# Kernel tuning notes

Measured on AMD Instinct MI355X. Metric: run time of the kernel, lower is better.

Reference implementation:

```python
import jax, jax.numpy as jnp
import numpy as np
import math

B, S, D, H, DFF = 2, 2048, 1024, 16, 4096
DK = D // H
EPS = 1e-6


def setup_inputs() -> dict:
    key = jax.random.key(0)
    ks = jax.random.split(key, 12)
    s = 0.02
    return {
        "x": jax.random.normal(ks[0], (B, S, D), jnp.float32),
        "mask": jnp.ones((B, S), jnp.int32),
        "wq": jax.random.normal(ks[1], (D, D), jnp.float32) * s,
        "bq": jnp.zeros((D,), jnp.float32),
        "wk": jax.random.normal(ks[2], (D, D), jnp.float32) * s,
        "bk": jnp.zeros((D,), jnp.float32),
        "wv": jax.random.normal(ks[3], (D, D), jnp.float32) * s,
        "bv": jnp.zeros((D,), jnp.float32),
        "wo": jax.random.normal(ks[4], (D, D), jnp.float32) * s,
        "bo": jnp.zeros((D,), jnp.float32),
        "g1": jnp.ones((D,), jnp.float32),
        "b1": jnp.zeros((D,), jnp.float32),
        "g2": jnp.ones((D,), jnp.float32),
        "b2": jnp.zeros((D,), jnp.float32),
        "w1": jax.random.normal(ks[5], (DFF, D), jnp.float32) * s,
        "bf1": jnp.zeros((DFF,), jnp.float32),
        "w2": jax.random.normal(ks[6], (D, DFF), jnp.float32) * s,
        "bf2": jnp.zeros((D,), jnp.float32),
    }


def _gelu(x):
    # x * 0.5 * (1 + erf(x / sqrt(2))) -- exact erf-based GELU as in source
    return x * 0.5 * (1.0 + jax.lax.erf(x * (1.0 / math.sqrt(2.0))))


def _layernorm(x, gamma, beta):
    # torch.std uses unbiased (ddof=1); eps is OUTSIDE the sqrt in the source
    mean = jnp.mean(x, axis=-1, keepdims=True)
    std = jnp.std(x, axis=-1, keepdims=True, ddof=1)
    return gamma * (x - mean) / (std + EPS) + beta


def _block(x, mask, wq, bq, wk, bk, wv, bv, wo, bo, g1, b1, g2, b2, w1, bf1, w2, bf2):
    # multi-head attention (dropout is identity in eval mode)
    q = (x @ wq.T + bq).reshape(B, S, H, DK).transpose(0, 2, 1, 3)  # bhsd
    k = (x @ wk.T + bk).reshape(B, S, H, DK).transpose(0, 2, 1, 3)
    v = (x @ wv.T + bv).reshape(B, S, H, DK).transpose(0, 2, 1, 3)
    scores = jnp.einsum("bhsd,bhtd->bhst", q, k) / math.sqrt(DK)
    scores = jnp.where(mask[:, None, None, :] == 0, -1e9, scores)
    attn = jax.nn.softmax(scores, axis=-1)
    cv = jnp.einsum("bhst,bhtd->bhsd", attn, v)
    cv = cv.transpose(0, 2, 1, 3).reshape(B, S, D)
    hd = cv @ wo.T + bo
    # residual + norm1
    hd = _layernorm(x + hd, g1, b1)
    # position-wise FFN with erf GELU
    ff = _gelu(hd @ w1.T + bf1) @ w2.T + bf2
    return _layernorm(hd + ff, g2, b2)


def reference(x, mask, wq, bq, wk, bk, wv, bv, wo, bo, g1, b1, g2, b2, w1, bf1, w2, bf2):
    return _block(x, mask, wq, bq, wk, bk, wv, bv, wo, bo, g1, b1, g2, b2, w1, bf1, w2, bf2)
```

## Files before the change

kernel.cpp:

```cpp
#include <hip/hip_runtime.h>
#include <hip/hip_bf16.h>

#define B_   2
#define S_   2048
#define D_   1024
#define H_   16
#define DK_  64
#define DFF_ 4096
#define M_   (B_*S_)

typedef unsigned short u16;
typedef __attribute__((ext_vector_type(8))) short short8;
typedef __attribute__((ext_vector_type(4))) short bf16x4;
typedef __attribute__((ext_vector_type(4))) float floatx4;

__device__ __forceinline__ u16 f2bf(float f) {
    union { float f; unsigned u; } v; v.f = f;
    unsigned r = v.u + 0x7fffu + ((v.u >> 16) & 1u);
    return (u16)(r >> 16);
}
__device__ __forceinline__ u16 f2bf_fast(float f) {
    __hip_bfloat16 h = __float2bfloat16(f);
    return *reinterpret_cast<u16*>(&h);
}
__device__ __forceinline__ float exp2_fast(float f) {
    return __builtin_amdgcn_exp2f(f);
}
__device__ __forceinline__ void g2l16(const u16* g, u16* l) {
    __builtin_amdgcn_global_load_lds((const __attribute__((address_space(1))) void*)g,
                                     (__attribute__((address_space(3))) void*)l,
                                     16, 0, 0);
}
__device__ __forceinline__ unsigned lds_off(const void* p) {
    return (unsigned)(unsigned long long)p;
}

#define TRB16(dst, va, IMM)                                                    \
    asm volatile("ds_read_b64_tr_b16 %0, %1 offset:" #IMM                      \
                 : "=v"(dst) : "v"(va))

__global__ __launch_bounds__(256) void cvt_all(
    const float* __restrict__ x,  const float* __restrict__ wq,
    const float* __restrict__ wk, const float* __restrict__ wv,
    const float* __restrict__ wo, const float* __restrict__ w1,
    const float* __restrict__ w2,
    u16* __restrict__ xb, u16* __restrict__ wqkvb, u16* __restrict__ wob,
    u16* __restrict__ w1b, u16* __restrict__ w2b) {
    for (int i = blockIdx.x * 256 + threadIdx.x; i < 4194304;
         i += gridDim.x * 256) {
        const float* s; u16* d; int off;
        if (i < 1048576)      { s = x;  d = xb;    off = i; }
        else if (i < 1310720) { s = wq; d = wqkvb; off = i - 1048576; }
        else if (i < 1572864) { s = wk; d = wqkvb + 1048576; off = i - 1310720; }
        else if (i < 1835008) { s = wv; d = wqkvb + 2097152; off = i - 1572864; }
        else if (i < 2097152) { s = wo; d = wob;   off = i - 1835008; }
        else if (i < 3145728) { s = w1; d = w1b;   off = i - 2097152; }
        else                  { s = w2; d = w2b;   off = i - 3145728; }
        float4 v = reinterpret_cast<const float4*>(s)[off];
        ushort4 o;
        o.x = f2bf(v.x); o.y = f2bf(v.y); o.z = f2bf(v.z); o.w = f2bf(v.w);
        reinterpret_cast<ushort4*>(d)[off] = o;
    }
}

__global__ __launch_bounds__(256) void prep_misc(const float* __restrict__ bq,
                                                 const float* __restrict__ bk,
                                                 const float* __restrict__ bv,
                                                 const int* __restrict__ mask,
                                                 float* __restrict__ bqkv,
                                                 float* __restrict__ mbias) {
    int i = blockIdx.x * 256 + threadIdx.x;
    if (i < 3 * D_) {
        float v = (i < D_) ? bq[i] : (i < 2 * D_) ? bk[i - D_] : bv[i - 2 * D_];
        bqkv[i] = v;
    } else if (i < 3 * D_ + B_ * S_) {
        int k = i - 3 * D_;
        mbias[k] = (mask[k] == 0) ? -1.44269504e9f : 0.0f;
    }
}

template <int EPI>
__global__ __launch_bounds__(512, 2) void gemm256_bt(const u16* __restrict__ A,
                                                     const u16* __restrict__ Bw,
                                                     const float* __restrict__ bias,
                                                     u16* __restrict__ Cb,
                                                     float* __restrict__ Cf,
                                                     int N, int K) {
    __shared__ alignas(16) u16 sA[2][2][8192];
    __shared__ alignas(16) u16 sB[2][2][8192];
    const int tid = threadIdx.x;
    const int wid = tid >> 6, lane = tid & 63;
    const int lrow = lane & 15, lgrp = lane >> 4;
    const int wm = wid >> 2, wn = wid & 3;
    const int z = blockIdx.z;
    const int Kc = K / gridDim.z;
    const int zbase = z * Kc;

    const int nbx = gridDim.x, nby = gridDim.y;
    const int nwg = nbx * nby;
    const int orig = blockIdx.y * nbx + blockIdx.x;
    const int qd = nwg >> 3, rr = nwg & 7, xc = orig & 7, oi = orig >> 3;
    const int swz = (xc < rr ? xc * (qd + 1) : rr * (qd + 1) + (xc - rr) * qd) + oi;
    const int m0 = (swz / nby) * 256, n0 = (swz % nby) * 256;

    const u16* Ab = A + (size_t)m0 * K + zbase;
    const u16* Bb = Bw + (size_t)n0 * K + zbase;
    const int T = Kc >> 6;

    const int c0 = (wid * 2 + 0) * 64 + lane;
    const int c1 = (wid * 2 + 1) * 64 + lane;
    const int r0 = c0 >> 3, g0 = c0 & 7;
    const int r1 = c1 >> 3, g1 = c1 & 7;
    const size_t so0 = (size_t)r0 * K + (size_t)((g0 ^ (r0 & 7)) * 8);
    const size_t so1 = (size_t)r1 * K + (size_t)((g1 ^ (r1 & 7)) * 8);
    const int d0 = (wid * 2 + 0) * 512;
    const int d1 = (wid * 2 + 1) * 512;

    auto stageA = [&](int par, int half, int kt) {
        const u16* src = Ab + (size_t)(half * 128) * K + kt * 64;
        g2l16(src + so0, &sA[par][half][d0]);
        g2l16(src + so1, &sA[par][half][d1]);
    };
    auto stageB = [&](int par, int half, int kt) {
        const u16* src = Bb + (size_t)(half * 128) * K + kt * 64;
        g2l16(src + so0, &sB[par][half][d0]);
        g2l16(src + so1, &sB[par][half][d1]);
    };

    stageA(0, 0, 0); stageA(0, 1, 0);
    stageB(0, 0, 0); stageB(0, 1, 0);
    if (T > 1) { stageB(1, 0, 1); stageB(1, 1, 1); }
    asm volatile("s_waitcnt vmcnt(4)" ::: "memory");
    asm volatile("s_barrier" ::: "memory");

    floatx4 acc[8][4] = {};
    const int rbase = (wn & 1) * 64;
    const int bhalf = wn >> 1;

    for (int t = 0; t < T; t++) {
        const int par = t & 1;
        const char* baseA = (const char*)&sA[par][wm][0];
        const char* baseB = (const char*)&sB[par][bhalf][0];
        short8 bfr[4][2];
#pragma unroll
        for (int ph = 0; ph < 4; ph++) {
            if (ph == 0) {
#pragma unroll
                for (int nj = 0; nj < 4; nj++) {
                    int rb = rbase + nj * 16 + lrow;
#pragma unroll
                    for (int kk = 0; kk < 2; kk++) {
                        int off = rb * 128 + (((kk * 4 + lgrp) ^ (lrow & 7)) * 16);
                        bfr[nj][kk] = *reinterpret_cast<const short8*>(baseB + off);
                    }
                }
            }
            short8 af[2][2];
#pragma unroll
            for (int a = 0; a < 2; a++) {
                int ra = (2 * ph + a) * 16 + lrow;
#pragma unroll
                for (int kk = 0; kk < 2; kk++) {
                    int off = ra * 128 + (((kk * 4 + lgrp) ^ (lrow & 7)) * 16);
                    af[a][kk] = *reinterpret_cast<const short8*>(baseA + off);
                }
            }
            if (ph == 0) { if (t + 1 < T) stageA(par ^ 1, 0, t + 1); }
            if (ph == 1) { if (t + 1 < T) stageA(par ^ 1, 1, t + 1); }
            if (ph == 2) { if (t + 2 < T) stageB(par, 0, t + 2); }
            if (ph == 3) { if (t + 2 < T) stageB(par, 1, t + 2); }

            asm volatile("s_barrier" ::: "memory");
            asm volatile("s_waitcnt lgkmcnt(0)" ::: "memory");
            __builtin_amdgcn_sched_barrier(0);

            __builtin_amdgcn_s_setprio(1);
#pragma unroll
            for (int a = 0; a < 2; a++)
#pragma unroll
                for (int nj = 0; nj < 4; nj++) {
                    acc[2 * ph + a][nj] = __builtin_amdgcn_mfma_f32_16x16x32_bf16(
                        af[a][0], bfr[nj][0], acc[2 * ph + a][nj], 0, 0, 0);
                    acc[2 * ph + a][nj] = __builtin_amdgcn_mfma_f32_16x16x32_bf16(
                        af[a][1], bfr[nj][1], acc[2 * ph + a][nj], 0, 0, 0);
                }
            __builtin_amdgcn_s_setprio(0);

            if (ph == 3) {
                if (t >= T - 3) asm volatile("s_waitcnt vmcnt(0)" ::: "memory");
                else            asm volatile("s_waitcnt vmcnt(4)" ::: "memory");
            }
            asm volatile("s_barrier" ::: "memory");
        }
    }

    float* Co = (EPI == 1) ? Cf + (size_t)z * M_ * N : nullptr;
#pragma unroll
    for (int mi = 0; mi < 8; mi++) {
        int row = m0 + wm * 128 + mi * 16 + lgrp * 4;
#pragma unroll
        for (int nj = 0; nj < 4; nj++) {
            int col = n0 + wn * 64 + nj * 16 + lrow;
            float bc = (EPI != 1 || z == 0) ? bias[col] : 0.0f;
#pragma unroll
            for (int j = 0; j < 4; j++) {
                float v = acc[mi][nj][j] + bc;
                if (EPI == 2) v = 0.5f * v * (1.0f + erff(v * 0.70710678118654752f));
                if (EPI == 1)
                    Co[(size_t)(row + j) * N + col] = v;
                else
                    Cb[(size_t)(row + j) * N + col] = f2bf(v);
            }
        }
    }
}

__global__ __launch_bounds__(512) void attn_kernel(const u16* __restrict__ QKV,
                                                   const float* __restrict__ mbias,
                                                   u16* __restrict__ O) {
    const int SD = 3 * D_;
    __shared__ alignas(16) u16 ktL[2][4096];
    __shared__ alignas(16) u16 vtL[2][4096];
    __shared__ alignas(16) u16 pL[8][1024];

    const int orig = blockIdx.y * gridDim.x + blockIdx.x;
    const int swz = (orig & 7) * 64 + (orig >> 3);
    const int qt = swz & 15, bh = swz >> 4;
    const int b = bh >> 4, h = bh & 15;

    const int tid = threadIdx.x, wid = tid >> 6, lane = tid & 63;
    const int lrow = lane & 15, lgrp = lane >> 4;

    const u16* Qp = QKV + h * DK_;
    const u16* Kp = QKV + D_ + h * DK_;
    const u16* Vp = QKV + 2 * D_ + h * DK_;
    const float* mbrow = mbias + b * S_;

    const int qr = qt * 128 + wid * 16 + lrow;
    const u16* qrow = Qp + (size_t)(b * S_ + qr) * SD;
    short8 aq0 = *reinterpret_cast<const short8*>(qrow + lgrp * 8);
    short8 aq1 = *reinterpret_cast<const short8*>(qrow + 32 + lgrp * 8);

    const int q8 = wid * 64 + lane;
    const int krow = q8 >> 3, kcb = q8 & 7;
    const u16* kq = Kp + (size_t)(b * S_ + krow) * SD + ((kcb ^ (krow & 7)) * 8);
    const int ov = wid * 512 + lane * 8;
    const int vk = ((ov >> 6) & 7) * 8 + ((ov >> 9) & 1) * 4 + ((ov >> 4) & 3);
    const int vd = (ov >> 10) * 16 + (ov & 8);
    const u16* vq = Vp + (size_t)(b * S_ + vk) * SD + vd;

    auto issue = [&](int bufIdx) {
        g2l16(kq, &ktL[bufIdx][wid * 512]);
        g2l16(vq, &vtL[bufIdx][wid * 512]);
        kq += 64 * SD;
        vq += 64 * SD;
    };

    floatx4 accO[4] = {};
    float mrun = -1e30f, lrun = 0.f;
    const float SC2 = 0.18033688011112042f;

    issue(0);
    int cur = 0;
    for (int t = 0; t < S_ / 64; t++) {
        const int kv0 = t * 64;
        if (t < S_ / 64 - 1) {
            issue(cur ^ 1);
            asm volatile("s_waitcnt vmcnt(2)" ::: "memory");
        } else {
            asm volatile("s_waitcnt vmcnt(0)" ::: "memory");
        }
        __builtin_amdgcn_s_barrier();
        asm volatile("" ::: "memory");

        const u16* ktc = ktL[cur];
        const unsigned vva = lds_off(vtL[cur]) + lane * 8;

        float4 mb[4];
#pragma unroll
        for (int ni = 0; ni < 4; ni++)
            mb[ni] = *reinterpret_cast<const float4*>(mbrow + kv0 + ni * 16 + lgrp * 4);

        floatx4 st[4];
        __builtin_amdgcn_s_setprio(1);
#pragma unroll
        for (int ni = 0; ni < 4; ni++) {
            int row = ni * 16 + lrow;
            int off0 = (row * 128 + lgrp * 16) ^ ((lrow & 7) << 4);
            int off1 = (row * 128 + 64 + lgrp * 16) ^ ((lrow & 7) << 4);
            short8 bk0 = *reinterpret_cast<const short8*>((const char*)ktc + off0);
            short8 bk1 = *reinterpret_cast<const short8*>((const char*)ktc + off1);
            floatx4 z = {0.f, 0.f, 0.f, 0.f};
            z = __builtin_amdgcn_mfma_f32_16x16x32_bf16(bk0, aq0, z, 0, 0, 0);
            z = __builtin_amdgcn_mfma_f32_16x16x32_bf16(bk1, aq1, z, 0, 0, 0);
            st[ni] = z;
        }
        __builtin_amdgcn_s_setprio(0);

        bf16x4 vt0[4], vt1[4], vt2[4], vt3[4];
#pragma unroll
        for (int nd = 0; nd < 4; nd++) {
            unsigned a = vva + nd * 2048;
            TRB16(vt0[nd], a, 0);
            TRB16(vt1[nd], a, 1024);
            TRB16(vt2[nd], a, 512);
            TRB16(vt3[nd], a, 1536);
        }

        float pm[4][4];
#pragma unroll
        for (int ni = 0; ni < 4; ni++) {
            const float* mbp = reinterpret_cast<const float*>(&mb[ni]);
#pragma unroll
            for (int j = 0; j < 4; j++)
                pm[ni][j] = fmaf(st[ni][j], SC2, mbp[j]);
        }
        float pmax = pm[0][0];
#pragma unroll
        for (int ni = 0; ni < 4; ni++)
#pragma unroll
            for (int j = 0; j < 4; j++) pmax = fmaxf(pmax, pm[ni][j]);
        pmax = fmaxf(pmax, __shfl_xor(pmax, 16, 64));
        pmax = fmaxf(pmax, __shfl_xor(pmax, 32, 64));

        bool upd = !__all(pmax - mrun <= 11.5f);
        float fac = 1.0f;
        if (upd) {
            float mn = fmaxf(mrun, pmax);
            fac = exp2_fast(mrun - mn);
            mrun = mn;
        }

        float p[4][4];
        float s = 0.f;
#pragma unroll
        for (int ni = 0; ni < 4; ni++)
#pragma unroll
            for (int j = 0; j < 4; j++) {
                float e = exp2_fast(pm[ni][j] - mrun);
                p[ni][j] = e;
                s += e;
            }
        s += __shfl_xor(s, 16, 64);
        s += __shfl_xor(s, 32, 64);
        lrun = lrun * fac + s;

#pragma unroll
        for (int ni = 0; ni < 4; ni++) {
            bf16x4 pw;
#pragma unroll
            for (int j = 0; j < 4; j++) pw[j] = (short)f2bf_fast(p[ni][j]);
            unsigned woff = (unsigned)((lrow * 128 + ni * 32 + lgrp * 8) ^ ((lrow & 7) << 4));
            *reinterpret_cast<bf16x4*>((char*)pL[wid] + woff) = pw;
        }

        if (upd) {
            float f0 = __shfl(fac, lgrp * 4 + 0, 64);
            float f1 = __shfl(fac, lgrp * 4 + 1, 64);
            float f2 = __shfl(fac, lgrp * 4 + 2, 64);
            float f3 = __shfl(fac, lgrp * 4 + 3, 64);
#pragma unroll
            for (int nd = 0; nd < 4; nd++) {
                floatx4 tt = accO[nd];
                tt[0] *= f0; tt[1] *= f1; tt[2] *= f2; tt[3] *= f3;
                accO[nd] = tt;
            }
        }

        asm volatile("s_waitcnt lgkmcnt(0)" ::: "memory");
        __builtin_amdgcn_sched_barrier(0);

        unsigned ra0 = (unsigned)((lrow * 128 + lgrp * 16) ^ ((lrow & 7) << 4));
        unsigned ra1 = (unsigned)((lrow * 128 + 64 + lgrp * 16) ^ ((lrow & 7) << 4));
        short8 ap0 = *reinterpret_cast<const short8*>((const char*)pL[wid] + ra0);
        short8 ap1 = *reinterpret_cast<const short8*>((const char*)pL[wid] + ra1);

        __builtin_amdgcn_s_setprio(1);
#pragma unroll
        for (int nd = 0; nd < 4; nd++) {
            short8 bv0 = __builtin_shufflevector(vt0[nd], vt1[nd], 0, 1, 2, 3, 4, 5, 6, 7);
            short8 bv1 = __builtin_shufflevector(vt2[nd], vt3[nd], 0, 1, 2, 3, 4, 5, 6, 7);
            accO[nd] = __builtin_amdgcn_mfma_f32_16x16x32_bf16(ap0, bv0, accO[nd], 0, 0, 0);
            accO[nd] = __builtin_amdgcn_mfma_f32_16x16x32_bf16(ap1, bv1, accO[nd], 0, 0, 0);
        }
        __builtin_amdgcn_s_setprio(0);

        asm volatile("" ::: "memory");
        __builtin_amdgcn_s_barrier();
        cur ^= 1;
    }

    float linv = 1.0f / lrun;
    float li[4];
#pragma unroll
    for (int j = 0; j < 4; j++) li[j] = __shfl(linv, lgrp * 4 + j, 64);
#pragma unroll
    for (int nd = 0; nd < 4; nd++)
#pragma unroll
        for (int j = 0; j < 4; j++) {
            int r = lgrp * 4 + j;
            float v = accO[nd][j] * li[j];
            O[(size_t)(b * S_ + qt * 128 + wid * 16 + r) * D_ + h * DK_ + nd * 16 + lrow] =
                f2bf_fast(v);
        }
}

template <int NR>
__global__ __launch_bounds__(256) void ln_kernel(const float* __restrict__ X,
                                                 const float* __restrict__ R0,
                                                 const float* __restrict__ R1,
                                                 const float* __restrict__ R2,
                                                 const float* __restrict__ R3,
                                                 const float* __restrict__ gam,
                                                 const float* __restrict__ bet,
                                                 float* __restrict__ outf,
                                                 u16* __restrict__ outb) {
    __shared__ float ws1[4], ws2[4];
    const int row = blockIdx.x, tid = threadIdx.x;
    const size_t ro = (size_t)row * D_;
    float4 v = reinterpret_cast<const float4*>(X + ro)[tid];
    {
        const float4 r = reinterpret_cast<const float4*>(R0 + ro)[tid];
        v.x += r.x; v.y += r.y; v.z += r.z; v.w += r.w;
    }
    if (NR >= 2) {
        const float4 r = reinterpret_cast<const float4*>(R1 + ro)[tid];
        v.x += r.x; v.y += r.y; v.z += r.z; v.w += r.w;
    }
    if (NR >= 3) {
        const float4 r = reinterpret_cast<const float4*>(R2 + ro)[tid];
        v.x += r.x; v.y += r.y; v.z += r.z; v.w += r.w;
    }
    if (NR >= 4) {
        const float4 r = reinterpret_cast<const float4*>(R3 + ro)[tid];
        v.x += r.x; v.y += r.y; v.z += r.z; v.w += r.w;
    }

    float s = v.x + v.y + v.z + v.w;
#pragma unroll
    for (int m = 32; m >= 1; m >>= 1) s += __shfl_xor(s, m, 64);
    if ((tid & 63) == 0) ws1[tid >> 6] = s;
    __syncthreads();
    float mean = (ws1[0] + ws1[1] + ws1[2] + ws1[3]) * (1.f / D_);

    float4 d; d.x = v.x - mean; d.y = v.y - mean; d.z = v.z - mean; d.w = v.w - mean;
    float q = d.x * d.x + d.y * d.y + d.z * d.z + d.w * d.w;
#pragma unroll
    for (int m = 32; m >= 1; m >>= 1) q += __shfl_xor(q, m, 64);
    if ((tid & 63) == 0) ws2[tid >> 6] = q;
    __syncthreads();
    float var = (ws2[0] + ws2[1] + ws2[2] + ws2[3]) * (1.f / (D_ - 1));
    float inv = 1.f / (sqrtf(var) + 1e-6f);

    const float4 g = reinterpret_cast<const float4*>(gam)[tid];
    const float4 bb = reinterpret_cast<const float4*>(bet)[tid];
    float4 o;
    o.x = g.x * d.x * inv + bb.x;
    o.y = g.y * d.y * inv + bb.y;
    o.z = g.z * d.z * inv + bb.z;
    o.w = g.w * d.w * inv + bb.w;
    if (outf) reinterpret_cast<float4*>(outf + ro)[tid] = o;
    if (outb) {
        ushort4 ob;
        ob.x = f2bf(o.x); ob.y = f2bf(o.y); ob.z = f2bf(o.z); ob.w = f2bf(o.w);
        reinterpret_cast<ushort4*>(outb + ro)[tid] = ob;
    }
}

extern "C" void kernel_launch(void* const* d_in, const int* in_sizes, int n_in,
                              void* d_out, int out_size, void* d_ws, size_t ws_size,
                              hipStream_t stream) {
    const float* x    = (const float*)d_in[0];
    const int*   mask = (const int*)d_in[1];
    const float* wq   = (const float*)d_in[2];
    const float* bq   = (const float*)d_in[3];
    const float* wk   = (const float*)d_in[4];
    const float* bk   = (const float*)d_in[5];
    const float* wv   = (const float*)d_in[6];
    const float* bv   = (const float*)d_in[7];
    const float* wo   = (const float*)d_in[8];
    const float* bo   = (const float*)d_in[9];
    const float* g1   = (const float*)d_in[10];
    const float* b1   = (const float*)d_in[11];
    const float* g2   = (const float*)d_in[12];
    const float* b2   = (const float*)d_in[13];
    const float* w1   = (const float*)d_in[14];
    const float* bf1  = (const float*)d_in[15];
    const float* w2   = (const float*)d_in[16];
    const float* bf2  = (const float*)d_in[17];
    float* out = (float*)d_out;

    char* ws = (char*)d_ws;
    const size_t MB = 1u << 20;
    u16*   xb    = (u16*)  (ws + 0 * MB);
    u16*   wqkvb = (u16*)  (ws + 8 * MB);
    u16*   qkvb  = (u16*)  (ws + 14 * MB);
    u16*   cvb   = (u16*)  (ws + 64 * MB);
    float* pp    = (float*)(ws + 0 * MB);
    float* qpart = (float*)(ws + 0 * MB);
    u16*   wob   = (u16*)  (ws + 72 * MB);
    u16*   w1b   = (u16*)  (ws + 74 * MB);
    u16*   w2b   = (u16*)  (ws + 82 * MB);
    float* bqkv  = (float*)(ws + 90 * MB);
    float* mbias = (float*)(ws + 90 * MB + 65536);
    float* hdf   = (float*)(ws + 91 * MB);
    u16*   hdb   = (u16*)  (ws + 107 * MB);
    u16*   ff1b  = (u16*)  (ws + 115 * MB);

    cvt_all<<<2048, 256, 0, stream>>>(x, wq, wk, wv, wo, w1, w2,
                                      xb, wqkvb, wob, w1b, w2b);
    prep_misc<<<28, 256, 0, stream>>>(bq, bk, bv, mask, bqkv, mbias);

    gemm256_bt<0><<<dim3(M_ / 256, 3 * D_ / 256, 1), 512, 0, stream>>>(
        xb, wqkvb, bqkv, qkvb, nullptr, 3 * D_, D_);

    attn_kernel<<<dim3(S_ / 128, B_ * H_), 512, 0, stream>>>(qkvb, mbias, cvb);

    gemm256_bt<1><<<dim3(M_ / 256, D_ / 256, 4), 512, 0, stream>>>(
        cvb, wob, bo, nullptr, pp, D_, D_);

    ln_kernel<4><<<M_, 256, 0, stream>>>(x, pp, pp + (size_t)M_ * D_,
                                         pp + 2 * (size_t)M_ * D_,
                                         pp + 3 * (size_t)M_ * D_,
                                         g1, b1, hdf, hdb);

    gemm256_bt<2><<<dim3(M_ / 256, DFF_ / 256, 1), 512, 0, stream>>>(
        hdb, w1b, bf1, ff1b, nullptr, DFF_, D_);

    gemm256_bt<1><<<dim3(M_ / 256, D_ / 256, 4), 512, 0, stream>>>(
        ff1b, w2b, bf2, nullptr, qpart, D_, DFF_);

    ln_kernel<4><<<M_, 256, 0, stream>>>(hdf, qpart, qpart + (size_t)M_ * D_,
                                         qpart + 2 * (size_t)M_ * D_,
                                         qpart + 3 * (size_t)M_ * D_,
                                         g2, b2, out, nullptr);
}
```

Measured before the change: 381.6 us.

## Store split-K partials in bf16, shrink attention blocks, merge prep kernels

The split-K GEMM partial sums are now written as bf16 instead of fp32, and the layernorm kernels read bf16 partials. This halves partial-sum write and read traffic at the cost of extra rounding error. The attention kernel moves from 128-row/512-thread blocks to 64-row/256-thread blocks, doubling the grid, with each wave issuing two K/V async loads per tile. The bias and mask prep kernel is folded into the conversion kernel, saving one launch.

```diff
diff --git a/kernel.cpp b/kernel.cpp
--- a/kernel.cpp
+++ b/kernel.cpp
@@ -23,6 +23,9 @@
     __hip_bfloat16 h = __float2bfloat16(f);
     return *reinterpret_cast<u16*>(&h);
 }
+__device__ __forceinline__ float b2f(u16 u) {
+    union { unsigned u; float f; } v; v.u = ((unsigned)u) << 16; return v.f;
+}
 __device__ __forceinline__ float exp2_fast(float f) {
     return __builtin_amdgcn_exp2f(f);
 }
@@ -44,38 +47,36 @@
     const float* __restrict__ wk, const float* __restrict__ wv,
     const float* __restrict__ wo, const float* __restrict__ w1,
     const float* __restrict__ w2,
+    const float* __restrict__ bq, const float* __restrict__ bk,
+    const float* __restrict__ bv, const int* __restrict__ mask,
     u16* __restrict__ xb, u16* __restrict__ wqkvb, u16* __restrict__ wob,
-    u16* __restrict__ w1b, u16* __restrict__ w2b) {
-    for (int i = blockIdx.x * 256 + threadIdx.x; i < 4194304;
+    u16* __restrict__ w1b, u16* __restrict__ w2b,
+    float* __restrict__ bqkv, float* __restrict__ mbias) {
+    for (int i = blockIdx.x * 256 + threadIdx.x; i < 4201472;
          i += gridDim.x * 256) {
-        const float* s; u16* d; int off;
-        if (i < 1048576)      { s = x;  d = xb;    off = i; }
-        else if (i < 1310720) { s = wq; d = wqkvb; off = i - 1048576; }
-        else if (i < 1572864) { s = wk; d = wqkvb + 1048576; off = i - 1310720; }
-        else if (i < 1835008) { s = wv; d = wqkvb + 2097152; off = i - 1572864; }
-        else if (i < 2097152) { s = wo; d = wob;   off = i - 1835008; }
-        else if (i < 3145728) { s = w1; d = w1b;   off = i - 2097152; }
-        else                  { s = w2; d = w2b;   off = i - 3145728; }
-        float4 v = reinterpret_cast<const float4*>(s)[off];
-        ushort4 o;
-        o.x = f2bf(v.x); o.y = f2bf(v.y); o.z = f2bf(v.z); o.w = f2bf(v.w);
-        reinterpret_cast<ushort4*>(d)[off] = o;
-    }
-}
-
-__global__ __launch_bounds__(256) void prep_misc(const float* __restrict__ bq,
-                                                 const float* __restrict__ bk,
-                                                 const float* __restrict__ bv,
-                                                 const int* __restrict__ mask,
-                                                 float* __restrict__ bqkv,
-                                                 float* __restrict__ mbias) {
-    int i = blockIdx.x * 256 + threadIdx.x;
-    if (i < 3 * D_) {
-        float v = (i < D_) ? bq[i] : (i < 2 * D_) ? bk[i - D_] : bv[i - 2 * D_];
-        bqkv[i] = v;
-    } else if (i < 3 * D_ + B_ * S_) {
-        int k = i - 3 * D_;
-        mbias[k] = (mask[k] == 0) ? -1.44269504e9f : 0.0f;
+        if (i < 4194304) {
+            const float* s; u16* d; int off;
+            if (i < 1048576)      { s = x;  d = xb;    off = i; }
+            else if (i < 1310720) { s = wq; d = wqkvb; off = i - 1048576; }
+            else if (i < 1572864) { s = wk; d = wqkvb + 1048576; off = i - 1310720; }
+            else if (i < 1835008) { s = wv; d = wqkvb + 2097152; off = i - 1572864; }
+            else if (i < 2097152) { s = wo; d = wob;   off = i - 1835008; }
+            else if (i < 3145728) { s = w1; d = w1b;   off = i - 2097152; }
+            else                  { s = w2; d = w2b;   off = i - 3145728; }
+            float4 v = reinterpret_cast<const float4*>(s)[off];
+            ushort4 o;
+            o.x = f2bf(v.x); o.y = f2bf(v.y); o.z = f2bf(v.z); o.w = f2bf(v.w);
+            reinterpret_cast<ushort4*>(d)[off] = o;
+        } else {
+            int j = i - 4194304;
+            if (j < 3 * D_) {
+                float v = (j < D_) ? bq[j] : (j < 2 * D_) ? bk[j - D_] : bv[j - 2 * D_];
+                bqkv[j] = v;
+            } else {
+                int k = j - 3 * D_;
+                mbias[k] = (mask[k] == 0) ? -1.44269504e9f : 0.0f;
+            }
+        }
     }
 }
 
@@ -84,7 +85,6 @@
                                                      const u16* __restrict__ Bw,
                                                      const float* __restrict__ bias,
                                                      u16* __restrict__ Cb,
-                                                     float* __restrict__ Cf,
                                                      int N, int K) {
     __shared__ alignas(16) u16 sA[2][2][8192];
     __shared__ alignas(16) u16 sB[2][2][8192];
@@ -194,7 +194,7 @@
         }
     }
 
-    float* Co = (EPI == 1) ? Cf + (size_t)z * M_ * N : nullptr;
+    u16* Co = (EPI == 1) ? Cb + (size_t)z * M_ * N : Cb;
 #pragma unroll
     for (int mi = 0; mi < 8; mi++) {
         int row = m0 + wm * 128 + mi * 16 + lgrp * 4;
@@ -206,26 +206,23 @@
             for (int j = 0; j < 4; j++) {
                 float v = acc[mi][nj][j] + bc;
                 if (EPI == 2) v = 0.5f * v * (1.0f + erff(v * 0.70710678118654752f));
-                if (EPI == 1)
-                    Co[(size_t)(row + j) * N + col] = v;
-                else
-                    Cb[(size_t)(row + j) * N + col] = f2bf(v);
-            }
-        }
-    }
-}
-
-__global__ __launch_bounds__(512) void attn_kernel(const u16* __restrict__ QKV,
+                Co[(size_t)(row + j) * N + col] = f2bf(v);
+            }
+        }
+    }
+}
+
+__global__ __launch_bounds__(256) void attn_kernel(const u16* __restrict__ QKV,
                                                    const float* __restrict__ mbias,
                                                    u16* __restrict__ O) {
     const int SD = 3 * D_;
     __shared__ alignas(16) u16 ktL[2][4096];
     __shared__ alignas(16) u16 vtL[2][4096];
-    __shared__ alignas(16) u16 pL[8][1024];
+    __shared__ alignas(16) u16 pL[4][1024];
 
     const int orig = blockIdx.y * gridDim.x + blockIdx.x;
-    const int swz = (orig & 7) * 64 + (orig >> 3);
-    const int qt = swz & 15, bh = swz >> 4;
+    const int swz = (orig & 7) * 128 + (orig >> 3);
+    const int qt = swz & 31, bh = swz >> 5;
     const int b = bh >> 4, h = bh & 15;
 
     const int tid = threadIdx.x, wid = tid >> 6, lane = tid & 63;
@@ -236,24 +233,36 @@
     const u16* Vp = QKV + 2 * D_ + h * DK_;
     const float* mbrow = mbias + b * S_;
 
-    const int qr = qt * 128 + wid * 16 + lrow;
+    const int qr = qt * 64 + wid * 16 + lrow;
     const u16* qrow = Qp + (size_t)(b * S_ + qr) * SD;
     short8 aq0 = *reinterpret_cast<const short8*>(qrow + lgrp * 8);
     short8 aq1 = *reinterpret_cast<const short8*>(qrow + 32 + lgrp * 8);
 
-    const int q8 = wid * 64 + lane;
-    const int krow = q8 >> 3, kcb = q8 & 7;
-    const u16* kq = Kp + (size_t)(b * S_ + krow) * SD + ((kcb ^ (krow & 7)) * 8);
-    const int ov = wid * 512 + lane * 8;
-    const int vk = ((ov >> 6) & 7) * 8 + ((ov >> 9) & 1) * 4 + ((ov >> 4) & 3);
-    const int vd = (ov >> 10) * 16 + (ov & 8);
-    const u16* vq = Vp + (size_t)(b * S_ + vk) * SD + vd;
+    const u16* kq[2];
+    const u16* vq[2];
+#pragma unroll
+    for (int i = 0; i < 2; i++) {
+        int s = wid * 2 + i;
+        int q8 = s * 64 + lane;
+        int krow = q8 >> 3, kcb = q8 & 7;
+        kq[i] = Kp + (size_t)(b * S_ + krow) * SD + ((kcb ^ (krow & 7)) * 8);
+        int o = s * 512 + lane * 8;
+        int vk = ((o >> 6) & 7) * 8 + ((o >> 9) & 1) * 4 + ((o >> 4) & 3);
+        int vd = (o >> 10) * 16 + (o & 8);
+        vq[i] = Vp + (size_t)(b * S_ + vk) * SD + vd;
+    }
 
     auto issue = [&](int bufIdx) {
-        g2l16(kq, &ktL[bufIdx][wid * 512]);
-        g2l16(vq, &vtL[bufIdx][wid * 512]);
-        kq += 64 * SD;
-        vq += 64 * SD;
+        u16* kb_ = ktL[bufIdx];
+        u16* vb_ = vtL[bufIdx];
+#pragma unroll
+        for (int i = 0; i < 2; i++) {
+            int s = wid * 2 + i;
+            g2l16(kq[i], kb_ + s * 512);
+            g2l16(vq[i], vb_ + s * 512);
+            kq[i] += 64 * SD;
+            vq[i] += 64 * SD;
+        }
     };
 
     floatx4 accO[4] = {};
@@ -266,7 +275,7 @@
         const int kv0 = t * 64;
         if (t < S_ / 64 - 1) {
             issue(cur ^ 1);
-            asm volatile("s_waitcnt vmcnt(2)" ::: "memory");
+            asm volatile("s_waitcnt vmcnt(4)" ::: "memory");
         } else {
             asm volatile("s_waitcnt vmcnt(0)" ::: "memory");
         }
@@ -400,40 +409,39 @@
         for (int j = 0; j < 4; j++) {
             int r = lgrp * 4 + j;
             float v = accO[nd][j] * li[j];
-            O[(size_t)(b * S_ + qt * 128 + wid * 16 + r) * D_ + h * DK_ + nd * 16 + lrow] =
+            O[(size_t)(b * S_ + qt * 64 + wid * 16 + r) * D_ + h * DK_ + nd * 16 + lrow] =
                 f2bf_fast(v);
         }
 }
 
-template <int NR>
-__global__ __launch_bounds__(256) void ln_kernel(const float* __restrict__ X,
-                                                 const float* __restrict__ R0,
-                                                 const float* __restrict__ R1,
-                                                 const float* __restrict__ R2,
-                                                 const float* __restrict__ R3,
-                                                 const float* __restrict__ gam,
-                                                 const float* __restrict__ bet,
-                                                 float* __restrict__ outf,
-                                                 u16* __restrict__ outb) {
+__global__ __launch_bounds__(256) void ln_bf(const float* __restrict__ X,
+                                             const u16* __restrict__ R0,
+                                             const u16* __restrict__ R1,
+                                             const u16* __restrict__ R2,
+                                             const u16* __restrict__ R3,
+                                             const float* __restrict__ gam,
+                                             const float* __restrict__ bet,
+                                             float* __restrict__ outf,
+                                             u16* __restrict__ outb) {
     __shared__ float ws1[4], ws2[4];
     const int row = blockIdx.x, tid = threadIdx.x;
     const size_t ro = (size_t)row * D_;
     float4 v = reinterpret_cast<const float4*>(X + ro)[tid];
     {
-        const float4 r = reinterpret_cast<const float4*>(R0 + ro)[tid];
-        v.x += r.x; v.y += r.y; v.z += r.z; v.w += r.w;
-    }
-    if (NR >= 2) {
-        const float4 r = reinterpret_cast<const float4*>(R1 + ro)[tid];
-        v.x += r.x; v.y += r.y; v.z += r.z; v.w += r.w;
-    }
-    if (NR >= 3) {
-        const float4 r = reinterpret_cast<const float4*>(R2 + ro)[tid];
-        v.x += r.x; v.y += r.y; v.z += r.z; v.w += r.w;
-    }
-    if (NR >= 4) {
-        const float4 r = reinterpret_cast<const float4*>(R3 + ro)[tid];
-        v.x += r.x; v.y += r.y; v.z += r.z; v.w += r.w;
+        ushort4 r = reinterpret_cast<const ushort4*>(R0 + ro)[tid];
+        v.x += b2f(r.x); v.y += b2f(r.y); v.z += b2f(r.z); v.w += b2f(r.w);
+    }
+    {
+        ushort4 r = reinterpret_cast<const ushort4*>(R1 + ro)[tid];
+        v.x += b2f(r.x); v.y += b2f(r.y); v.z += b2f(r.z); v.w += b2f(r.w);
+    }
+    {
+        ushort4 r = reinterpret_cast<const ushort4*>(R2 + ro)[tid];
+        v.x += b2f(r.x); v.y += b2f(r.y); v.z += b2f(r.z); v.w += b2f(r.w);
+    }
+    {
+        ushort4 r = reinterpret_cast<const ushort4*>(R3 + ro)[tid];
+        v.x += b2f(r.x); v.y += b2f(r.y); v.z += b2f(r.z); v.w += b2f(r.w);
     }
 
     float s = v.x + v.y + v.z + v.w;
@@ -496,8 +504,8 @@
     u16*   wqkvb = (u16*)  (ws + 8 * MB);
     u16*   qkvb  = (u16*)  (ws + 14 * MB);
     u16*   cvb   = (u16*)  (ws + 64 * MB);
-    float* pp    = (float*)(ws + 0 * MB);
-    float* qpart = (float*)(ws + 0 * MB);
+    u16*   pp    = (u16*)  (ws + 0 * MB);
+    u16*   qpart = (u16*)  (ws + 0 * MB);
     u16*   wob   = (u16*)  (ws + 72 * MB);
     u16*   w1b   = (u16*)  (ws + 74 * MB);
     u16*   w2b   = (u16*)  (ws + 82 * MB);
@@ -508,30 +516,30 @@
     u16*   ff1b  = (u16*)  (ws + 115 * MB);
 
     cvt_all<<<2048, 256, 0, stream>>>(x, wq, wk, wv, wo, w1, w2,
-                                      xb, wqkvb, wob, w1b, w2b);
-    prep_misc<<<28, 256, 0, stream>>>(bq, bk, bv, mask, bqkv, mbias);
+                                      bq, bk, bv, mask,
+                                      xb, wqkvb, wob, w1b, w2b, bqkv, mbias);
 
     gemm256_bt<0><<<dim3(M_ / 256, 3 * D_ / 256, 1), 512, 0, stream>>>(
-        xb, wqkvb, bqkv, qkvb, nullptr, 3 * D_, D_);
-
-    attn_kernel<<<dim3(S_ / 128, B_ * H_), 512, 0, stream>>>(qkvb, mbias, cvb);
+        xb, wqkvb, bqkv, qkvb, 3 * D_, D_);
+
+    attn_kernel<<<dim3(S_ / 64, B_ * H_), 256, 0, stream>>>(qkvb, mbias, cvb);
 
     gemm256_bt<1><<<dim3(M_ / 256, D_ / 256, 4), 512, 0, stream>>>(
-        cvb, wob, bo, nullptr, pp, D_, D_);
-
-    ln_kernel<4><<<M_, 256, 0, stream>>>(x, pp, pp + (size_t)M_ * D_,
-                                         pp + 2 * (size_t)M_ * D_,
-                                         pp + 3 * (size_t)M_ * D_,
-                                         g1, b1, hdf, hdb);
+        cvb, wob, bo, pp, D_, D_);
+
+    ln_bf<<<M_, 256, 0, stream>>>(x, pp, pp + (size_t)M_ * D_,
+                                  pp + 2 * (size_t)M_ * D_,
+                                  pp + 3 * (size_t)M_ * D_,
+                                  g1, b1, hdf, hdb);
 
     gemm256_bt<2><<<dim3(M_ / 256, DFF_ / 256, 1), 512, 0, stream>>>(
-        hdb, w1b, bf1, ff1b, nullptr, DFF_, D_);
+        hdb, w1b, bf1, ff1b, DFF_, D_);
 
     gemm256_bt<1><<<dim3(M_ / 256, D_ / 256, 4), 512, 0, stream>>>(
-        ff1b, w2b, bf2, nullptr, qpart, D_, DFF_);
-
-    ln_kernel<4><<<M_, 256, 0, stream>>>(hdf, qpart, qpart + (size_t)M_ * D_,
-                                         qpart + 2 * (size_t)M_ * D_,
-                                         qpart + 3 * (size_t)M_ * D_,
-                                         g2, b2, out, nullptr);
-}
+        ff1b, w2b, bf2, qpart, D_, DFF_);
+
+    ln_bf<<<M_, 256, 0, stream>>>(hdf, qpart, qpart + (size_t)M_ * D_,
+                                  qpart + 2 * (size_t)M_ * D_,
+                                  qpart + 3 * (size_t)M_ * D_,
+                                  g2, b2, out, nullptr);
+}
```

Measured after the change: 408.1 us. 6.9% more time.
